# Performance work log

Hardware: AMD Instinct MI355X
Metric: run time of the kernel (lower is better)

## Reference

```python
import jax, jax.numpy as jnp
import numpy as np
from jax import lax

EPS = 1e-4  # BatchNorm eps from the module
K = 3       # kernel_size
PAD = 1     # padding


def setup_inputs() -> dict:
    key = jax.random.key(0)
    k1, k2, k3 = jax.random.split(key, 3)
    N, Cin, H, Wd = 32, 256, 56, 56
    Cout = 256
    x = jax.random.normal(k1, (N, Cin, H, Wd), dtype=jnp.float32)
    gamma = jnp.ones((Cin,), dtype=jnp.float32)
    beta_bn = jnp.zeros((Cin,), dtype=jnp.float32)
    W = jax.random.normal(k2, (Cout, Cin, K, K), dtype=jnp.float32) * 0.05
    b = jax.random.normal(k3, (Cout,), dtype=jnp.float32) * 0.01
    return {"x": x, "gamma": gamma, "beta_bn": beta_bn, "W": W, "b": b}


def _conv(x, w, padding):
    return lax.conv_general_dilated(
        x, w, window_strides=(1, 1),
        padding=[(padding, padding), (padding, padding)],
        dimension_numbers=("NCHW", "OIHW", "NCHW"))


def reference(x, gamma, beta_bn, W, b):
    # BatchNorm2d in training mode: batch statistics over (N, H, W), biased var
    mu = jnp.mean(x, axis=(0, 2, 3), keepdims=True)
    var = jnp.var(x, axis=(0, 2, 3), keepdims=True)
    xn = (x - mu) * lax.rsqrt(var + EPS)
    xn = xn * gamma[None, :, None, None] + beta_bn[None, :, None, None]

    # BinActiv: per-pixel channel-mean of |x|, then sign-binarize
    m = jnp.mean(jnp.abs(xn), axis=1, keepdims=True)  # [N,1,H,W]
    xb = jnp.sign(xn)

    # Binarize weights; alpha = L1 norm per output filter / n
    n = W.shape[1] * W.shape[2] * W.shape[3]
    alpha = jnp.sum(jnp.abs(W), axis=(1, 2, 3)) / n  # [Cout]
    Wb = jnp.sign(W)

    y = _conv(xb, Wb, PAD) + b[None, :, None, None]

    # beta map: box filter (stride 1) over channel-mean magnitudes
    box = jnp.full((1, 1, K, K), 1.0 / (K * K), dtype=x.dtype)
    beta_map = _conv(m, box, PAD)  # [N,1,Ho,Wo]

    out = jax.nn.relu(y * beta_map * alpha[None, :, None, None])
    return out
```

## Files before the change

### kernel.cpp

```cpp
#include <hip/hip_runtime.h>
#include <cstdint>
#include <cstddef>

#define N_    32
#define C_    256
#define H_    56
#define W_    56
#define HW_   (H_ * W_)
#define NHW_  (N_ * HW_)
#define COUT_ 256
#define EPS_  1e-4f
#define PW_   58
#define PIMG_ (PW_ * PW_)

__global__ void k_bn_partial(const float* __restrict__ x,
                             float* __restrict__ ps, float* __restrict__ pq) {
    const int c = blockIdx.x >> 3;
    const int s = blockIdx.x & 7;
    const int t = threadIdx.x;
    float sm = 0.f, sq = 0.f;
    for (int n = s * 4; n < s * 4 + 4; ++n) {
        const float4* p = (const float4*)(x + (size_t)(n * C_ + c) * HW_);
        for (int i = t; i < HW_ / 4; i += 256) {
            float4 v = p[i];
            sm += v.x + v.y + v.z + v.w;
            sq += v.x * v.x + v.y * v.y + v.z * v.z + v.w * v.w;
        }
    }
    __shared__ float ls[256], lq[256];
    ls[t] = sm; lq[t] = sq;
    __syncthreads();
    for (int off = 128; off >= 1; off >>= 1) {
        if (t < off) { ls[t] += ls[t + off]; lq[t] += lq[t + off]; }
        __syncthreads();
    }
    if (t == 0) { ps[s * C_ + c] = ls[0]; pq[s * C_ + c] = lq[0]; }
}

__global__ void k_bn_final(const float* __restrict__ ps, const float* __restrict__ pq,
                           const float* __restrict__ gamma, const float* __restrict__ beta,
                           float* __restrict__ a, float* __restrict__ bb) {
    const int c = threadIdx.x;
    float sm = 0.f, sq = 0.f;
    for (int s = 0; s < 8; ++s) { sm += ps[s * C_ + c]; sq += pq[s * C_ + c]; }
    float mu   = sm * (1.f / NHW_);
    float var  = sq * (1.f / NHW_) - mu * mu;
    float rstd = rsqrtf(var + EPS_);
    float g    = gamma[c] * rstd;
    a[c]  = g;
    bb[c] = beta[c] - mu * g;
}

__global__ void k_wpack(const float* __restrict__ Wt, float* __restrict__ alpha,
                        uint64_t* __restrict__ wbits, int* __restrict__ ctab) {
    const int co = blockIdx.x;
    const int ci = threadIdx.x;
    const int lane = ci & 63, wave = ci >> 6;
    const float* p = Wt + (size_t)(co * C_ + ci) * 9;
    float wv[9];
    float asum = 0.f;
#pragma unroll
    for (int t = 0; t < 9; ++t) { wv[t] = p[t]; asum += fabsf(wv[t]); }
    __shared__ int Pl[9];
    if (ci < 9) Pl[ci] = 0;
    __syncthreads();
#pragma unroll
    for (int t = 0; t < 9; ++t) {
        uint64_t mask = __ballot(wv[t] > 0.f);
        if (lane == 0) {
            wbits[(co * 9 + t) * 4 + wave] = mask;
            atomicAdd(&Pl[t], (int)__popcll(mask));
        }
    }
    __shared__ float red[256];
    red[ci] = asum;
    __syncthreads();
    for (int off = 128; off >= 1; off >>= 1) {
        if (ci < off) red[ci] += red[ci + off];
        __syncthreads();
    }
    if (ci == 0) alpha[co] = red[0] * (1.f / 2304.f);
    if (ci < 9) {
        const int rc = ci / 3, cc = ci % 3;
        unsigned m9 = (rc == 0 ? 0x007u : 0u) | (rc == 2 ? 0x1C0u : 0u)
                    | (cc == 0 ? 0x049u : 0u) | (cc == 2 ? 0x124u : 0u);
        int s = 0;
#pragma unroll
        for (int t = 0; t < 9; ++t)
            if ((m9 >> t) & 1) s += 2 * Pl[t] - 256;
        ctab[ci * 256 + co] = s;
    }
}

__global__ void k_mpack(const float* __restrict__ x, const float* __restrict__ a,
                        const float* __restrict__ bb, uint64_t* __restrict__ xbits,
                        float* __restrict__ m) {
    const int p = blockIdx.x * 256 + threadIdx.x;
    const int n = p / HW_;
    const int hw = p - n * HW_;
    const int h = hw / W_;
    const int w = hw - h * W_;
    const float* xp = x + (size_t)n * C_ * HW_ + hw;
    float macc = 0.f;
    uint64_t bits[4];
#pragma unroll
    for (int wd = 0; wd < 4; ++wd) {
        uint64_t bw = 0;
#pragma unroll
        for (int j = 0; j < 64; ++j) {
            const int c = wd * 64 + j;
            float xn = fmaf(xp[(size_t)c * HW_], a[c], bb[c]);
            macc += fabsf(xn);
            bw |= (xn > 0.f) ? (1ull << j) : 0ull;
        }
        bits[wd] = bw;
    }
    ulonglong2* xb = (ulonglong2*)(xbits + ((size_t)n * PIMG_ + (size_t)(h + 1) * PW_ + (w + 1)) * 4);
    xb[0] = make_ulonglong2(bits[0], bits[1]);
    xb[1] = make_ulonglong2(bits[2], bits[3]);
    m[p] = macc * (1.f / C_);
}

__global__ void k_box(const float* __restrict__ m, float* __restrict__ beta_map) {
    const int idx = blockIdx.x * 256 + threadIdx.x;
    if (idx >= NHW_) return;
    const int w = idx % W_;
    const int h = (idx / W_) % H_;
    const int n = idx / HW_;
    const float* mp = m + (size_t)n * HW_;
    float s = 0.f;
#pragma unroll
    for (int dh = 0; dh < 3; ++dh) {
        int ih = h + dh - 1;
        if (ih < 0 || ih >= H_) continue;
#pragma unroll
        for (int dw = 0; dw < 3; ++dw) {
            int iw = w + dw - 1;
            if (iw < 0 || iw >= W_) continue;
            s += mp[ih * W_ + iw];
        }
    }
    beta_map[idx] = s * (1.f / 9.f);
}

__global__ void __launch_bounds__(256, 4)
k_conv(const uint64_t* __restrict__ xbits, const uint64_t* __restrict__ wbits,
       const int* __restrict__ ctab, const float* __restrict__ beta_map,
       const float* __restrict__ alpha, const float* __restrict__ bias,
       float* __restrict__ out) {
    const int p   = blockIdx.x * 256 + (int)threadIdx.x;
    const int grp = blockIdx.y;
    const int n  = p / HW_;
    const int hw = p - n * HW_;
    const int h  = hw / W_;
    const int w  = hw - h * W_;

    const uint64_t* xb = xbits + ((size_t)n * PIMG_ + (size_t)h * PW_ + w) * 4;
    uint64_t xw[36];
#pragma unroll
    for (int dh = 0; dh < 3; ++dh)
#pragma unroll
        for (int dw = 0; dw < 3; ++dw) {
            const uint64_t* tp = xb + ((size_t)dh * PW_ + dw) * 4;
#pragma unroll
            for (int wd = 0; wd < 4; ++wd)
                xw[(dh * 3 + dw) * 4 + wd] = tp[wd];
        }

    const int rowcls = (h == 0) ? 0 : ((h == H_ - 1) ? 2 : 1);
    const int colcls = (w == 0) ? 0 : ((w == W_ - 1) ? 2 : 1);
    const int* crow = ctab + (rowcls * 3 + colcls) * 256 + grp * 64;

    const float bm = beta_map[p];
    float* op = out + (size_t)n * COUT_ * HW_ + (size_t)(grp * 64) * HW_ + hw;

    for (int coi = 0; coi < 64; ++coi) {
        const int co = grp * 64 + coi;
        const uint64_t* wq = wbits + (size_t)co * 36;
        int a0 = 0, a1 = 0, a2 = 0, a3 = 0;
#pragma unroll
        for (int t = 0; t < 9; ++t) {
            a0 += __popcll(xw[t * 4 + 0] ^ wq[t * 4 + 0]);
            a1 += __popcll(xw[t * 4 + 1] ^ wq[t * 4 + 1]);
            a2 += __popcll(xw[t * 4 + 2] ^ wq[t * 4 + 2]);
            a3 += __popcll(xw[t * 4 + 3] ^ wq[t * 4 + 3]);
        }
        const int acc = (a0 + a1) + (a2 + a3);
        const int dot = 2304 - 2 * acc + crow[coi];
        float o = ((float)dot + bias[co]) * bm * alpha[co];
        o = fmaxf(o, 0.f);
        op[(size_t)coi * HW_] = o;
    }
}

extern "C" void kernel_launch(void* const* d_in, const int* in_sizes, int n_in,
                              void* d_out, int out_size, void* d_ws, size_t ws_size,
                              hipStream_t stream) {
    (void)in_sizes; (void)n_in; (void)out_size; (void)ws_size;
    const float* x     = (const float*)d_in[0];
    const float* gamma = (const float*)d_in[1];
    const float* betab = (const float*)d_in[2];
    const float* Wt    = (const float*)d_in[3];
    const float* b     = (const float*)d_in[4];
    float* out = (float*)d_out;

    uint8_t* base = (uint8_t*)d_ws;
    float*    ps       = (float*)(base + 0);
    float*    pq       = (float*)(base + 8192);
    float*    a        = (float*)(base + 16384);
    float*    bb       = (float*)(base + 17408);
    float*    alpha    = (float*)(base + 18432);
    int*      ctab     = (int*)(base + 19456);
    uint64_t* wbits    = (uint64_t*)(base + 28672);
    uint64_t* xbits    = (uint64_t*)(base + 102400);
    float*    m        = (float*)(base + 3547136);
    float*    beta_map = (float*)(base + 3948544);

    k_bn_partial<<<2048, 256, 0, stream>>>(x, ps, pq);
    k_bn_final<<<1, 256, 0, stream>>>(ps, pq, gamma, betab, a, bb);
    k_wpack<<<COUT_, 256, 0, stream>>>(Wt, alpha, wbits, ctab);
    hipMemsetAsync(xbits, 0, (size_t)N_ * PIMG_ * 4 * sizeof(uint64_t), stream);
    k_mpack<<<NHW_ / 256, 256, 0, stream>>>(x, a, bb, xbits, m);
    k_box<<<(NHW_ + 255) / 256, 256, 0, stream>>>(m, beta_map);
    k_conv<<<dim3(NHW_ / 256, 4), 256, 0, stream>>>(xbits, wbits, ctab, beta_map, alpha, b, out);
}
```

Measured before the change: 337.0 us.

## Remap binary conv to thread-per-output-channel with LDS-staged tile stores

The XNOR-popcount conv now assigns one output channel per thread. Each thread keeps its channel's packed weight bits in registers, and the block walks 32 consecutive pixels whose input bit words are uniform broadcast loads. Results go through a shared-memory tile so each channel writes contiguous float4 runs, replacing the per-pixel scattered weight reads. The bit-packing kernel is also split so each of four waves handles 64 channels of a 64-pixel group, with the |x| means combined in shared memory. This raises parallelism in the packing pass, at the cost of heavier register use (lower launch-bounds occupancy) and a shared-memory transpose in the conv.

```diff
diff --git a/kernel.cpp b/kernel.cpp
--- a/kernel.cpp
+++ b/kernel.cpp
@@ -12,6 +12,7 @@
 #define EPS_  1e-4f
 #define PW_   58
 #define PIMG_ (PW_ * PW_)
+#define TPX_  32
 
 __global__ void k_bn_partial(const float* __restrict__ x,
                              float* __restrict__ ps, float* __restrict__ pq) {
@@ -95,30 +96,35 @@
 __global__ void k_mpack(const float* __restrict__ x, const float* __restrict__ a,
                         const float* __restrict__ bb, uint64_t* __restrict__ xbits,
                         float* __restrict__ m) {
-    const int p = blockIdx.x * 256 + threadIdx.x;
-    const int n = p / HW_;
+    const int lane = (int)(threadIdx.x & 63);
+    const int wd   = (int)(threadIdx.x >> 6);
+    const int p  = blockIdx.x * 64 + lane;
+    const int n  = p / HW_;
     const int hw = p - n * HW_;
-    const int h = hw / W_;
-    const int w = hw - h * W_;
-    const float* xp = x + (size_t)n * C_ * HW_ + hw;
-    float macc = 0.f;
-    uint64_t bits[4];
-#pragma unroll
-    for (int wd = 0; wd < 4; ++wd) {
-        uint64_t bw = 0;
-#pragma unroll
-        for (int j = 0; j < 64; ++j) {
-            const int c = wd * 64 + j;
-            float xn = fmaf(xp[(size_t)c * HW_], a[c], bb[c]);
-            macc += fabsf(xn);
-            bw |= (xn > 0.f) ? (1ull << j) : 0ull;
-        }
-        bits[wd] = bw;
-    }
-    ulonglong2* xb = (ulonglong2*)(xbits + ((size_t)n * PIMG_ + (size_t)(h + 1) * PW_ + (w + 1)) * 4);
-    xb[0] = make_ulonglong2(bits[0], bits[1]);
-    xb[1] = make_ulonglong2(bits[2], bits[3]);
-    m[p] = macc * (1.f / C_);
+    const int h  = hw / W_;
+    const int w  = hw - h * W_;
+    const float* xp = x + ((size_t)(n * C_ + wd * 64)) * HW_ + hw;
+    float m0 = 0.f, m1 = 0.f, m2 = 0.f, m3 = 0.f;
+    uint64_t bw = 0;
+#pragma unroll
+    for (int j = 0; j < 64; j += 4) {
+#pragma unroll
+        for (int k = 0; k < 4; ++k) {
+            const int c = wd * 64 + j + k;
+            float xn = fmaf(xp[(size_t)(j + k) * HW_], a[c], bb[c]);
+            if (k == 0) m0 += fabsf(xn); else if (k == 1) m1 += fabsf(xn);
+            else if (k == 2) m2 += fabsf(xn); else m3 += fabsf(xn);
+            bw |= (xn > 0.f) ? (1ull << (j + k)) : 0ull;
+        }
+    }
+    xbits[((size_t)n * PIMG_ + (size_t)(h + 1) * PW_ + (w + 1)) * 4 + wd] = bw;
+    __shared__ float ms[4][64];
+    ms[wd][lane] = (m0 + m1) + (m2 + m3);
+    __syncthreads();
+    if (threadIdx.x < 64) {
+        float s = (ms[0][lane] + ms[1][lane]) + (ms[2][lane] + ms[3][lane]);
+        m[p] = s * (1.f / C_);
+    }
 }
 
 __global__ void k_box(const float* __restrict__ m, float* __restrict__ beta_map) {
@@ -143,53 +149,59 @@
     beta_map[idx] = s * (1.f / 9.f);
 }
 
-__global__ void __launch_bounds__(256, 4)
+__global__ void __launch_bounds__(256, 3)
 k_conv(const uint64_t* __restrict__ xbits, const uint64_t* __restrict__ wbits,
        const int* __restrict__ ctab, const float* __restrict__ beta_map,
        const float* __restrict__ alpha, const float* __restrict__ bias,
        float* __restrict__ out) {
-    const int p   = blockIdx.x * 256 + (int)threadIdx.x;
-    const int grp = blockIdx.y;
-    const int n  = p / HW_;
-    const int hw = p - n * HW_;
-    const int h  = hw / W_;
-    const int w  = hw - h * W_;
-
-    const uint64_t* xb = xbits + ((size_t)n * PIMG_ + (size_t)h * PW_ + w) * 4;
-    uint64_t xw[36];
-#pragma unroll
-    for (int dh = 0; dh < 3; ++dh)
-#pragma unroll
-        for (int dw = 0; dw < 3; ++dw) {
-            const uint64_t* tp = xb + ((size_t)dh * PW_ + dw) * 4;
-#pragma unroll
-            for (int wd = 0; wd < 4; ++wd)
-                xw[(dh * 3 + dw) * 4 + wd] = tp[wd];
-        }
-
-    const int rowcls = (h == 0) ? 0 : ((h == H_ - 1) ? 2 : 1);
-    const int colcls = (w == 0) ? 0 : ((w == W_ - 1) ? 2 : 1);
-    const int* crow = ctab + (rowcls * 3 + colcls) * 256 + grp * 64;
-
-    const float bm = beta_map[p];
-    float* op = out + (size_t)n * COUT_ * HW_ + (size_t)(grp * 64) * HW_ + hw;
-
-    for (int coi = 0; coi < 64; ++coi) {
-        const int co = grp * 64 + coi;
-        const uint64_t* wq = wbits + (size_t)co * 36;
-        int a0 = 0, a1 = 0, a2 = 0, a3 = 0;
-#pragma unroll
-        for (int t = 0; t < 9; ++t) {
-            a0 += __popcll(xw[t * 4 + 0] ^ wq[t * 4 + 0]);
-            a1 += __popcll(xw[t * 4 + 1] ^ wq[t * 4 + 1]);
-            a2 += __popcll(xw[t * 4 + 2] ^ wq[t * 4 + 2]);
-            a3 += __popcll(xw[t * 4 + 3] ^ wq[t * 4 + 3]);
-        }
-        const int acc = (a0 + a1) + (a2 + a3);
-        const int dot = 2304 - 2 * acc + crow[coi];
-        float o = ((float)dot + bias[co]) * bm * alpha[co];
-        o = fmaxf(o, 0.f);
-        op[(size_t)coi * HW_] = o;
+    const int t   = (int)threadIdx.x;
+    const int p0  = blockIdx.x * TPX_;
+    const int n   = p0 / HW_;
+    const int hw0 = p0 - n * HW_;
+
+    uint64_t wreg[36];
+    {
+        const uint64_t* wp = wbits + (size_t)t * 36;
+#pragma unroll
+        for (int i = 0; i < 36; ++i) wreg[i] = wp[i];
+    }
+    const float al = alpha[t];
+    const float bv = bias[t];
+
+    __shared__ float tile[256][TPX_ + 1];
+
+    const uint64_t* xim = xbits + (size_t)n * PIMG_ * 4;
+
+    for (int i = 0; i < TPX_; ++i) {
+        const int hw = hw0 + i;
+        const int h  = hw / W_;
+        const int w  = hw - h * W_;
+        int acc = 0;
+#pragma unroll
+        for (int dh = 0; dh < 3; ++dh) {
+            const uint64_t* row = xim + ((size_t)(h + dh) * PW_ + w) * 4;
+            uint64_t xs[12];
+#pragma unroll
+            for (int j = 0; j < 12; ++j) xs[j] = row[j];
+#pragma unroll
+            for (int j = 0; j < 12; ++j)
+                acc += __popcll(xs[j] ^ wreg[dh * 12 + j]);
+        }
+        const int rowcls = (h == 0) ? 0 : ((h == H_ - 1) ? 2 : 1);
+        const int colcls = (w == 0) ? 0 : ((w == W_ - 1) ? 2 : 1);
+        const int corr = ctab[(rowcls * 3 + colcls) * 256 + t];
+        const float bm = beta_map[p0 + i];
+        const int dot = 2304 - 2 * acc + corr;
+        float o = ((float)dot + bv) * bm * al;
+        tile[t][i] = fmaxf(o, 0.f);
+    }
+    __syncthreads();
+    float* op = out + ((size_t)(n * COUT_ + t)) * HW_ + hw0;
+#pragma unroll
+    for (int k = 0; k < TPX_ / 4; ++k) {
+        float4 v = make_float4(tile[t][4 * k], tile[t][4 * k + 1],
+                               tile[t][4 * k + 2], tile[t][4 * k + 3]);
+        ((float4*)op)[k] = v;
     }
 }
 
@@ -220,7 +232,7 @@
     k_bn_final<<<1, 256, 0, stream>>>(ps, pq, gamma, betab, a, bb);
     k_wpack<<<COUT_, 256, 0, stream>>>(Wt, alpha, wbits, ctab);
     hipMemsetAsync(xbits, 0, (size_t)N_ * PIMG_ * 4 * sizeof(uint64_t), stream);
-    k_mpack<<<NHW_ / 256, 256, 0, stream>>>(x, a, bb, xbits, m);
+    k_mpack<<<NHW_ / 64, 256, 0, stream>>>(x, a, bb, xbits, m);
     k_box<<<(NHW_ + 255) / 256, 256, 0, stream>>>(m, beta_map);
-    k_conv<<<dim3(NHW_ / 256, 4), 256, 0, stream>>>(xbits, wbits, ctab, beta_map, alpha, b, out);
-}
+    k_conv<<<NHW_ / TPX_, 256, 0, stream>>>(xbits, wbits, ctab, beta_map, alpha, b, out);
+}
```

Result: slower. 344.7 us (+2.3%).
